# Performance work log

Measured on AMD Instinct MI355X. Metric: run time of the kernel, lower is better.

## Reference

```python
import jax, jax.numpy as jnp
import numpy as np

P, N, NF = 4, 871, 512            # num_meta_paths, node_size (hardcoded 871 in source), node_feature_size
XDIM = 116 * 116                   # x_proj input dim, hardcoded Linear(116*116, nf)
BETA, LAMBDA_WL, GAMMA = 0.1, 0.1, 0.1


def _xavier(k, shape):
    fan_in, fan_out = shape[0], shape[-1]
    bound = np.sqrt(6.0 / (fan_in + fan_out))
    return jax.random.uniform(k, shape, jnp.float32, -bound, bound)


def setup_inputs() -> dict:
    key = jax.random.key(0)
    ks = jax.random.split(key, 12)
    return {
        "z_stack": jax.random.normal(ks[0], (P, N, NF), jnp.float32),
        "x_orig": jax.random.normal(ks[1], (1, 116, 116), jnp.float32),
        "W": _xavier(ks[2], (N, 1)),
        "b": jax.random.uniform(ks[3], (N, 1), jnp.float32),
        "q": _xavier(ks[4], (N, NF)),
        "xp_w": _xavier(ks[5], (XDIM, NF)),
        "xp_b": jnp.zeros((NF,), jnp.float32),
        "w1": _xavier(ks[6], (2 * NF, 512)), "b1": jnp.zeros((512,), jnp.float32),
        "w2": _xavier(ks[7], (512, 256)), "b2": jnp.zeros((256,), jnp.float32),
        "w3": _xavier(ks[8], (256, 1)), "b3": jnp.zeros((1,), jnp.float32),
        "perm": jax.random.permutation(ks[9], N).astype(jnp.int32),
    }


def _mi_mlp(t, w1, b1, w2, b2, w3, b3):
    h = jax.nn.relu(t @ w1 + b1)
    h = jax.nn.relu(h @ w2 + b2)
    return h @ w3 + b3  # [N, 1]


def reference(z_stack, x_orig, W, b, q, xp_w, xp_b, w1, b1, w2, b2, w3, b3, perm):
    # --- vectorized form of the per-node loop:
    # score_p = mean_i( tanh(W_i * z[p,i,:] + b_i) . q_i )
    zt = jnp.tanh(W[None] * z_stack + b[None])            # [P,N,NF]
    scores = jnp.mean(jnp.sum(zt * q[None], axis=-1), axis=-1)  # [P]
    proportions = scores / jnp.sum(scores)
    attn = jax.nn.softmax(proportions)                    # [P] (no isomorphic pairs -> no overwrite)
    # layer_out_p = attn_p * z_p + z_p ; emb = sum_p layer_out_p
    emb = jnp.einsum('p,pnf->nf', 1.0 + attn, z_stack)    # [N,NF]
    # --- estimate_MI(x_orig, emb, mi_estimator_xz)
    x = jnp.broadcast_to(x_orig.reshape(1, -1), (N, XDIM))
    xh = x @ xp_w + xp_b                                  # [N,NF]
    t0 = jnp.concatenate([xh, emb], axis=1)               # [N,2NF]
    t1 = jnp.concatenate([xh, emb[perm]], axis=1)
    mi_lb = jnp.mean(_mi_mlp(t0, w1, b1, w2, b2, w3, b3)) - jnp.log(
        jnp.mean(jnp.exp(_mi_mlp(t1, w1, b1, w2, b2, w3, b3))) + 1e-8)
    I_XZ = jnp.clip(mi_lb, 0.0)
    # y_labels=None -> I_ZY = 0 ; empty isomorphic_pairs -> wl_loss = 0
    total_loss = I_XZ - BETA * 0.0 + LAMBDA_WL * 0.0 + GAMMA * jnp.sum(attn)
    return emb, total_loss
```

## Files before the change

### kernel.cpp

```cpp
#include <hip/hip_runtime.h>
#include <hip/hip_bf16.h>
#include <math.h>

#define NMETA  4
#define NNODE  871
#define NFEAT  512
#define XDIM   (116*116)
#define ZPLANE (NNODE*NFEAT)
#define NCHUNK 55
#define MT     55

#define WS_COEF   8
#define WS_CNT    12
#define WS_SPART  16
#define WS_C1P    256
#define WS_XHP    8448
#define WS_V      73984
#define WS_W1P    74856
#define WS_W2P    205928

typedef short v8s __attribute__((ext_vector_type(8)));
typedef float v4f __attribute__((ext_vector_type(4)));

static __device__ __forceinline__ short f2bf(float f) {
  __hip_bfloat16 h = __float2bfloat16(f);
  return *reinterpret_cast<short*>(&h);
}

__global__ __launch_bounds__(256) void k_front(const float* __restrict__ x,
                                               const float* __restrict__ xpw,
                                               const float* __restrict__ w1,
                                               const float* __restrict__ w2,
                                               const float* __restrict__ z,
                                               const float* __restrict__ W,
                                               const float* __restrict__ b,
                                               const float* __restrict__ q,
                                               float* __restrict__ ws,
                                               short* __restrict__ w1p,
                                               short* __restrict__ w2p) {
  const int blk = blockIdx.x;
  const int tid = threadIdx.x;
  if (blk < 128) {
    const int f4 = tid & 127;
    const int rp = tid >> 7;
    const int d0 = blk * 106;
    const int rows = min(106, XDIM - d0);
    __shared__ float xs[106];
    if (tid < rows) xs[tid] = x[d0 + tid];
    __syncthreads();
    float4 acc = {0.f, 0.f, 0.f, 0.f};
    const float4* xp4 = (const float4*)xpw;
#pragma unroll 4
    for (int r = rp; r < rows; r += 2) {
      const float xv = xs[r];
      const float4 w = xp4[(size_t)(d0 + r) * 128 + f4];
      acc.x += xv * w.x; acc.y += xv * w.y; acc.z += xv * w.z; acc.w += xv * w.w;
    }
    __shared__ float4 red4[128];
    if (rp) red4[f4] = acc;
    __syncthreads();
    if (!rp) {
      float4 o = red4[f4];
      o.x += acc.x; o.y += acc.y; o.z += acc.z; o.w += acc.w;
      ((float4*)(ws + WS_XHP + (size_t)blk * NFEAT))[f4] = o;
    }
  } else if (blk < 512) {
    const int base = (blk - 128) * 256 + tid;
#pragma unroll
    for (int it = 0; it < 4; ++it) {
      int t = base + it * 98304;
      if (t < 262144) {
        int j = t & 7; int r = t >> 3;
        int n15 = r & 15; r >>= 4;
        int quad = r & 3; r >>= 2;
        int nt = r & 31; int kb = r >> 5;
        int k = kb * 32 + quad * 8 + j;
        int n = nt * 16 + n15;
        w1p[t] = f2bf(w1[(size_t)(512 + k) * 512 + n]);
      } else {
        int o = t - 262144;
        int j = o & 7; int r = o >> 3;
        int n15 = r & 15; r >>= 4;
        int quad = r & 3; r >>= 2;
        int nt = r & 15; int kb = r >> 4;
        int k = kb * 32 + quad * 8 + j;
        int n = nt * 16 + n15;
        w2p[o] = f2bf(w2[(size_t)k * 256 + n]);
      }
    }
  } else {
    const int sblk = blk - 512;
    const int p = sblk / NCHUNK;
    const int chunk = sblk % NCHUNK;
    const int i0 = chunk * 16;
    const int i1 = min(i0 + 16, NNODE);
    const int f4 = tid & 127;
    const int ip = tid >> 7;
    float local = 0.f;
    for (int i = i0 + ip; i < i1; i += 2) {
      const float wi = W[i];
      const float bi = b[i];
      const float4 zr = ((const float4*)(z + ((size_t)p * NNODE + i) * NFEAT))[f4];
      const float4 qr = ((const float4*)(q + (size_t)i * NFEAT))[f4];
      local += tanhf(wi * zr.x + bi) * qr.x + tanhf(wi * zr.y + bi) * qr.y
             + tanhf(wi * zr.z + bi) * qr.z + tanhf(wi * zr.w + bi) * qr.w;
    }
    __shared__ float red[256];
    red[tid] = local;
    __syncthreads();
    for (int s = 128; s > 0; s >>= 1) {
      if (tid < s) red[tid] += red[tid + s];
      __syncthreads();
    }
    if (tid == 0) ws[WS_SPART + sblk] = red[0];
  }
}

__global__ __launch_bounds__(256) void k_prep(const float* __restrict__ xpb,
                                              const float* __restrict__ w1,
                                              const float* __restrict__ b1,
                                              float* __restrict__ ws) {
  const int tid = threadIdx.x;
  if (blockIdx.x < 16) {
    const int bk = blockIdx.x;
    __shared__ float xs[32];
    {
      const int f = tid & 31;
      const int pg = tid >> 5;
      float s = 0.f;
#pragma unroll 4
      for (int p = pg; p < 128; p += 8)
        s += ws[WS_XHP + (size_t)p * NFEAT + bk * 32 + f];
      __shared__ float red[256];
      red[tid] = s;
      __syncthreads();
      if (tid < 32) {
        float t2 = 0.f;
#pragma unroll
        for (int g = 0; g < 8; ++g) t2 += red[g * 32 + tid];
        xs[tid] = t2 + xpb[bk * 32 + tid];
      }
      __syncthreads();
    }
    const int j4 = tid & 127;
    const int fp = tid >> 7;
    float4 acc = {0.f, 0.f, 0.f, 0.f};
    const float4* w14 = (const float4*)w1;
#pragma unroll
    for (int ff = 0; ff < 16; ++ff) {
      const int f = bk * 32 + fp * 16 + ff;
      const float xv = xs[fp * 16 + ff];
      const float4 w = w14[(size_t)f * 128 + j4];
      acc.x += xv * w.x; acc.y += xv * w.y; acc.z += xv * w.z; acc.w += xv * w.w;
    }
    __shared__ float4 red2[128];
    if (fp) red2[j4] = acc;
    __syncthreads();
    if (!fp) {
      float4 o = red2[j4];
      o.x += acc.x; o.y += acc.y; o.z += acc.z; o.w += acc.w;
      if (bk == 0) {
        o.x += b1[j4 * 4 + 0]; o.y += b1[j4 * 4 + 1];
        o.z += b1[j4 * 4 + 2]; o.w += b1[j4 * 4 + 3];
      }
      ((float4*)(ws + WS_C1P + (size_t)bk * NFEAT))[j4] = o;
    }
  } else {
    __shared__ float sp[220];
    if (tid < 220) sp[tid] = ws[WS_SPART + tid];
    __syncthreads();
    if (tid == 0) {
      float sv[NMETA], sum = 0.f;
#pragma unroll
      for (int p = 0; p < NMETA; ++p) {
        float s = 0.f;
        for (int c = 0; c < NCHUNK; ++c) s += sp[p * NCHUNK + c];
        sv[p] = s / (float)NNODE;
        sum += sv[p];
      }
      float m = -1e30f;
#pragma unroll
      for (int p = 0; p < NMETA; ++p) { sv[p] = sv[p] / sum; m = fmaxf(m, sv[p]); }
      float es = 0.f;
#pragma unroll
      for (int p = 0; p < NMETA; ++p) { sv[p] = expf(sv[p] - m); es += sv[p]; }
#pragma unroll
      for (int p = 0; p < NMETA; ++p) ws[WS_COEF + p] = 1.f + sv[p] / es;
      *(unsigned int*)&ws[WS_CNT] = 0u;
    }
    for (int i = tid; i < NNODE; i += 256) ws[WS_V + i] = 0.f;
  }
}

__global__ __launch_bounds__(512) void k_fused(const float* __restrict__ z,
                                               float* __restrict__ ws,
                                               float* __restrict__ out,
                                               const short* __restrict__ w1p,
                                               const short* __restrict__ w2p,
                                               const float* __restrict__ b2,
                                               const float* __restrict__ w3,
                                               const float* __restrict__ b3) {
  __shared__ __align__(16) short embs[8192];
  __shared__ __align__(16) short h2a[8192];
  __shared__ float cs[512];
  __shared__ float rf0[512], rf1[512];
  const int tid = threadIdx.x;
  const int r0 = blockIdx.x * 16;

  {
    float a0 = 0.f;
#pragma unroll
    for (int k = 0; k < 16; ++k) a0 += ws[WS_C1P + k * 512 + tid];
    cs[tid] = a0;
  }
  const float c0 = ws[WS_COEF + 0], c1c = ws[WS_COEF + 1];
  const float c2 = ws[WS_COEF + 2], c3 = ws[WS_COEF + 3];

  const int oc = tid & 63;
  const float4* z4 = (const float4*)z;
  float4* out4 = (float4*)out;
#pragma unroll
  for (int t = 0; t < 2; ++t) {
    const int row = (tid >> 6) + 8 * t;
    const int gr = r0 + row;
    const int slot = oc * 16 + (row ^ (oc & 15));
    v8s h;
    if (gr < NNODE) {
      const int zi = gr * 128 + oc * 2;
      float4 a0 = z4[zi],               a1 = z4[zi + 1];
      float4 b0 = z4[NNODE*128 + zi],   b1 = z4[NNODE*128 + zi + 1];
      float4 d0 = z4[2*NNODE*128 + zi], d1 = z4[2*NNODE*128 + zi + 1];
      float4 e0 = z4[3*NNODE*128 + zi], e1 = z4[3*NNODE*128 + zi + 1];
      float4 r0v, r1v;
      r0v.x = c0*a0.x + c1c*b0.x + c2*d0.x + c3*e0.x;
      r0v.y = c0*a0.y + c1c*b0.y + c2*d0.y + c3*e0.y;
      r0v.z = c0*a0.z + c1c*b0.z + c2*d0.z + c3*e0.z;
      r0v.w = c0*a0.w + c1c*b0.w + c2*d0.w + c3*e0.w;
      r1v.x = c0*a1.x + c1c*b1.x + c2*d1.x + c3*e1.x;
      r1v.y = c0*a1.y + c1c*b1.y + c2*d1.y + c3*e1.y;
      r1v.z = c0*a1.z + c1c*b1.z + c2*d1.z + c3*e1.z;
      r1v.w = c0*a1.w + c1c*b1.w + c2*d1.w + c3*e1.w;
      out4[zi] = r0v;
      out4[zi + 1] = r1v;
      h[0] = f2bf(r0v.x); h[1] = f2bf(r0v.y); h[2] = f2bf(r0v.z); h[3] = f2bf(r0v.w);
      h[4] = f2bf(r1v.x); h[5] = f2bf(r1v.y); h[6] = f2bf(r1v.z); h[7] = f2bf(r1v.w);
    } else {
      h = (v8s){0,0,0,0,0,0,0,0};
    }
    *(v8s*)(embs + slot * 8) = h;
  }
  __syncthreads();

  const int lane = tid & 63, w = tid >> 6;
  const int n15 = lane & 15, quad = lane >> 4;
  v4f e[4];
#pragma unroll
  for (int ct = 0; ct < 4; ++ct) e[ct] = (v4f){0.f, 0.f, 0.f, 0.f};
#pragma unroll
  for (int kb = 0; kb < 16; ++kb) {
    const int koct = kb * 4 + quad;
    v8s a = *(const v8s*)(embs + (koct * 16 + (n15 ^ (koct & 15))) * 8);
    const short* B = w1p + kb * 16384 + w * 2048 + quad * 128 + n15 * 8;
#pragma unroll
    for (int ct = 0; ct < 4; ++ct) {
      v8s bb = *(const v8s*)(B + ct * 512);
      e[ct] = __builtin_amdgcn_mfma_f32_16x16x32_bf16(a, bb, e[ct], 0, 0, 0);
    }
  }
#pragma unroll
  for (int ct = 0; ct < 4; ++ct) {
    const int col = w * 64 + ct * 16 + n15;
    const int koct = col >> 3, j = col & 7;
#pragma unroll
    for (int r = 0; r < 4; ++r) {
      const int m = quad * 4 + r;
      h2a[(koct * 16 + (m ^ (koct & 15))) * 8 + j] = f2bf(fmaxf(e[ct][r] + cs[col], 0.f));
    }
  }
  __syncthreads();

  v4f g[2];
#pragma unroll
  for (int ct = 0; ct < 2; ++ct) g[ct] = (v4f){0.f, 0.f, 0.f, 0.f};
#pragma unroll
  for (int kb = 0; kb < 16; ++kb) {
    const int koct = kb * 4 + quad;
    v8s a = *(const v8s*)(h2a + (koct * 16 + (n15 ^ (koct & 15))) * 8);
    const short* B = w2p + kb * 8192 + w * 1024 + quad * 128 + n15 * 8;
#pragma unroll
    for (int ct = 0; ct < 2; ++ct) {
      v8s bb = *(const v8s*)(B + ct * 512);
      g[ct] = __builtin_amdgcn_mfma_f32_16x16x32_bf16(a, bb, g[ct], 0, 0, 0);
    }
  }
#pragma unroll
  for (int r = 0; r < 4; ++r) {
    float s = 0.f;
#pragma unroll
    for (int ct = 0; ct < 2; ++ct) {
      const int col = w * 32 + ct * 16 + n15;
      s += fmaxf(g[ct][r] + b2[col], 0.f) * w3[col];
    }
    s += __shfl_xor(s, 1);
    s += __shfl_xor(s, 2);
    s += __shfl_xor(s, 4);
    s += __shfl_xor(s, 8);
    const int grow = r0 + quad * 4 + r;
    if (n15 == 0 && grow < NNODE) atomicAdd(&ws[WS_V + grow], s);
  }

  __shared__ unsigned last;
  __syncthreads();
  if (tid == 0) {
    __threadfence();
    unsigned old = atomicAdd((unsigned int*)&ws[WS_CNT], 1u);
    last = (old == MT - 1) ? 1u : 0u;
  }
  __syncthreads();
  if (last) {
    const float bias = b3[0];
    float s0 = 0.f, s1 = 0.f;
    for (int i = tid; i < NNODE; i += 512) {
      float xv = __hip_atomic_load(&ws[WS_V + i], __ATOMIC_RELAXED,
                                   __HIP_MEMORY_SCOPE_AGENT) + bias;
      s0 += xv;
      s1 += expf(xv);
    }
    rf0[tid] = s0; rf1[tid] = s1;
    __syncthreads();
    for (int s = 256; s > 0; s >>= 1) {
      if (tid < s) { rf0[tid] += rf0[tid + s]; rf1[tid] += rf1[tid + s]; }
      __syncthreads();
    }
    if (tid == 0) {
      float m0 = rf0[0] / (float)NNODE;
      float m1 = rf1[0] / (float)NNODE;
      float mi = m0 - logf(m1 + 1e-8f);
      out[ZPLANE] = fmaxf(mi, 0.f) + 0.1f;
    }
  }
}

extern "C" void kernel_launch(void* const* d_in, const int* in_sizes, int n_in,
                              void* d_out, int out_size, void* d_ws, size_t ws_size,
                              hipStream_t stream) {
  const float* z   = (const float*)d_in[0];
  const float* x   = (const float*)d_in[1];
  const float* W   = (const float*)d_in[2];
  const float* b   = (const float*)d_in[3];
  const float* q   = (const float*)d_in[4];
  const float* xpw = (const float*)d_in[5];
  const float* xpb = (const float*)d_in[6];
  const float* w1  = (const float*)d_in[7];
  const float* b1  = (const float*)d_in[8];
  const float* w2  = (const float*)d_in[9];
  const float* b2  = (const float*)d_in[10];
  const float* w3  = (const float*)d_in[11];
  const float* b3  = (const float*)d_in[12];
  float* out = (float*)d_out;
  float* ws  = (float*)d_ws;

  short* w1p = (short*)(ws + WS_W1P);
  short* w2p = (short*)(ws + WS_W2P);

  k_front<<<732, 256, 0, stream>>>(x, xpw, w1, w2, z, W, b, q, ws, w1p, w2p);
  k_prep<<<17, 256, 0, stream>>>(xpb, w1, b1, ws);
  k_fused<<<MT, 512, 0, stream>>>(z, ws, out, w1p, w2p, b2, w3, b3);
}
```

Measured before the change: 131.9 us.

## Fold k_prep into k_fused, recomputing xh·w1 and attention per block

```diff
diff --git a/kernel.cpp b/kernel.cpp
--- a/kernel.cpp
+++ b/kernel.cpp
@@ -88,7 +88,7 @@
         w2p[o] = f2bf(w2[(size_t)k * 256 + n]);
       }
     }
-  } else {
+  } else if (blk < 732) {
     const int sblk = blk - 512;
     const int p = sblk / NCHUNK;
     const int chunk = sblk % NCHUNK;
@@ -113,82 +113,9 @@
       __syncthreads();
     }
     if (tid == 0) ws[WS_SPART + sblk] = red[0];
-  }
-}
-
-__global__ __launch_bounds__(256) void k_prep(const float* __restrict__ xpb,
-                                              const float* __restrict__ w1,
-                                              const float* __restrict__ b1,
-                                              float* __restrict__ ws) {
-  const int tid = threadIdx.x;
-  if (blockIdx.x < 16) {
-    const int bk = blockIdx.x;
-    __shared__ float xs[32];
-    {
-      const int f = tid & 31;
-      const int pg = tid >> 5;
-      float s = 0.f;
-#pragma unroll 4
-      for (int p = pg; p < 128; p += 8)
-        s += ws[WS_XHP + (size_t)p * NFEAT + bk * 32 + f];
-      __shared__ float red[256];
-      red[tid] = s;
-      __syncthreads();
-      if (tid < 32) {
-        float t2 = 0.f;
-#pragma unroll
-        for (int g = 0; g < 8; ++g) t2 += red[g * 32 + tid];
-        xs[tid] = t2 + xpb[bk * 32 + tid];
-      }
-      __syncthreads();
-    }
-    const int j4 = tid & 127;
-    const int fp = tid >> 7;
-    float4 acc = {0.f, 0.f, 0.f, 0.f};
-    const float4* w14 = (const float4*)w1;
-#pragma unroll
-    for (int ff = 0; ff < 16; ++ff) {
-      const int f = bk * 32 + fp * 16 + ff;
-      const float xv = xs[fp * 16 + ff];
-      const float4 w = w14[(size_t)f * 128 + j4];
-      acc.x += xv * w.x; acc.y += xv * w.y; acc.z += xv * w.z; acc.w += xv * w.w;
-    }
-    __shared__ float4 red2[128];
-    if (fp) red2[j4] = acc;
-    __syncthreads();
-    if (!fp) {
-      float4 o = red2[j4];
-      o.x += acc.x; o.y += acc.y; o.z += acc.z; o.w += acc.w;
-      if (bk == 0) {
-        o.x += b1[j4 * 4 + 0]; o.y += b1[j4 * 4 + 1];
-        o.z += b1[j4 * 4 + 2]; o.w += b1[j4 * 4 + 3];
-      }
-      ((float4*)(ws + WS_C1P + (size_t)bk * NFEAT))[j4] = o;
-    }
   } else {
-    __shared__ float sp[220];
-    if (tid < 220) sp[tid] = ws[WS_SPART + tid];
-    __syncthreads();
-    if (tid == 0) {
-      float sv[NMETA], sum = 0.f;
-#pragma unroll
-      for (int p = 0; p < NMETA; ++p) {
-        float s = 0.f;
-        for (int c = 0; c < NCHUNK; ++c) s += sp[p * NCHUNK + c];
-        sv[p] = s / (float)NNODE;
-        sum += sv[p];
-      }
-      float m = -1e30f;
-#pragma unroll
-      for (int p = 0; p < NMETA; ++p) { sv[p] = sv[p] / sum; m = fmaxf(m, sv[p]); }
-      float es = 0.f;
-#pragma unroll
-      for (int p = 0; p < NMETA; ++p) { sv[p] = expf(sv[p] - m); es += sv[p]; }
-#pragma unroll
-      for (int p = 0; p < NMETA; ++p) ws[WS_COEF + p] = 1.f + sv[p] / es;
-      *(unsigned int*)&ws[WS_CNT] = 0u;
-    }
     for (int i = tid; i < NNODE; i += 256) ws[WS_V + i] = 0.f;
+    if (tid == 0) *(unsigned int*)&ws[WS_CNT] = 0u;
   }
 }
 
@@ -199,22 +126,74 @@
                                                const short* __restrict__ w2p,
                                                const float* __restrict__ b2,
                                                const float* __restrict__ w3,
-                                               const float* __restrict__ b3) {
+                                               const float* __restrict__ b3,
+                                               const float* __restrict__ w1,
+                                               const float* __restrict__ b1,
+                                               const float* __restrict__ xpb) {
   __shared__ __align__(16) short embs[8192];
   __shared__ __align__(16) short h2a[8192];
   __shared__ float cs[512];
   __shared__ float rf0[512], rf1[512];
+  __shared__ float cf[4];
+  __shared__ float xs2[512];
+  __shared__ float spl[220];
+  __shared__ float4 redc[3][128];
   const int tid = threadIdx.x;
   const int r0 = blockIdx.x * 16;
 
+  if (tid < 220) spl[tid] = ws[WS_SPART + tid];
   {
-    float a0 = 0.f;
-#pragma unroll
-    for (int k = 0; k < 16; ++k) a0 += ws[WS_C1P + k * 512 + tid];
-    cs[tid] = a0;
-  }
-  const float c0 = ws[WS_COEF + 0], c1c = ws[WS_COEF + 1];
-  const float c2 = ws[WS_COEF + 2], c3 = ws[WS_COEF + 3];
+    float xv = xpb[tid];
+#pragma unroll 8
+    for (int p = 0; p < 128; ++p) xv += ws[WS_XHP + (size_t)p * NFEAT + tid];
+    xs2[tid] = xv;
+  }
+  __syncthreads();
+  if (tid == 0) {
+    float sv[NMETA], sum = 0.f;
+#pragma unroll
+    for (int p = 0; p < NMETA; ++p) {
+      float s = 0.f;
+      for (int c = 0; c < NCHUNK; ++c) s += spl[p * NCHUNK + c];
+      sv[p] = s / (float)NNODE;
+      sum += sv[p];
+    }
+    float m = -1e30f;
+#pragma unroll
+    for (int p = 0; p < NMETA; ++p) { sv[p] = sv[p] / sum; m = fmaxf(m, sv[p]); }
+    float es = 0.f;
+#pragma unroll
+    for (int p = 0; p < NMETA; ++p) { sv[p] = expf(sv[p] - m); es += sv[p]; }
+#pragma unroll
+    for (int p = 0; p < NMETA; ++p) cf[p] = 1.f + sv[p] / es;
+  }
+  const int j4 = tid & 127;
+  const int fp = tid >> 7;
+  float4 acc = {0.f, 0.f, 0.f, 0.f};
+  {
+    const float4* w14 = (const float4*)w1;
+#pragma unroll 4
+    for (int ff = 0; ff < 128; ++ff) {
+      const int f = fp * 128 + ff;
+      const float xvf = xs2[f];
+      const float4 wv = w14[(size_t)f * 128 + j4];
+      acc.x += xvf * wv.x; acc.y += xvf * wv.y; acc.z += xvf * wv.z; acc.w += xvf * wv.w;
+    }
+    if (fp) redc[fp - 1][j4] = acc;
+  }
+  __syncthreads();
+  if (!fp) {
+    float4 o = acc;
+#pragma unroll
+    for (int g = 0; g < 3; ++g) {
+      float4 t = redc[g][j4];
+      o.x += t.x; o.y += t.y; o.z += t.z; o.w += t.w;
+    }
+    o.x += b1[j4 * 4 + 0]; o.y += b1[j4 * 4 + 1];
+    o.z += b1[j4 * 4 + 2]; o.w += b1[j4 * 4 + 3];
+    ((float4*)cs)[j4] = o;
+  }
+  const float c0 = cf[0], c1c = cf[1], c2 = cf[2], c3 = cf[3];
 
   const int oc = tid & 63;
   const float4* z4 = (const float4*)z;
@@ -228,7 +207,7 @@
     if (gr < NNODE) {
       const int zi = gr * 128 + oc * 2;
       float4 a0 = z4[zi],               a1 = z4[zi + 1];
-      float4 b0 = z4[NNODE*128 + zi],   b1 = z4[NNODE*128 + zi + 1];
+      float4 b0 = z4[NNODE*128 + zi],   b1v = z4[NNODE*128 + zi + 1];
       float4 d0 = z4[2*NNODE*128 + zi], d1 = z4[2*NNODE*128 + zi + 1];
       float4 e0 = z4[3*NNODE*128 + zi], e1 = z4[3*NNODE*128 + zi + 1];
       float4 r0v, r1v;
@@ -236,10 +215,10 @@
       r0v.y = c0*a0.y + c1c*b0.y + c2*d0.y + c3*e0.y;
       r0v.z = c0*a0.z + c1c*b0.z + c2*d0.z + c3*e0.z;
       r0v.w = c0*a0.w + c1c*b0.w + c2*d0.w + c3*e0.w;
-      r1v.x = c0*a1.x + c1c*b1.x + c2*d1.x + c3*e1.x;
-      r1v.y = c0*a1.y + c1c*b1.y + c2*d1.y + c3*e1.y;
-      r1v.z = c0*a1.z + c1c*b1.z + c2*d1.z + c3*e1.z;
-      r1v.w = c0*a1.w + c1c*b1.w + c2*d1.w + c3*e1.w;
+      r1v.x = c0*a1.x + c1c*b1v.x + c2*d1.x + c3*e1.x;
+      r1v.y = c0*a1.y + c1c*b1v.y + c2*d1.y + c3*e1.y;
+      r1v.z = c0*a1.z + c1c*b1v.z + c2*d1.z + c3*e1.z;
+      r1v.w = c0*a1.w + c1c*b1v.w + c2*d1.w + c3*e1.w;
       out4[zi] = r0v;
       out4[zi + 1] = r1v;
       h[0] = f2bf(r0v.x); h[1] = f2bf(r0v.y); h[2] = f2bf(r0v.z); h[3] = f2bf(r0v.w);
@@ -363,7 +342,6 @@
   short* w1p = (short*)(ws + WS_W1P);
   short* w2p = (short*)(ws + WS_W2P);
 
-  k_front<<<732, 256, 0, stream>>>(x, xpw, w1, w2, z, W, b, q, ws, w1p, w2p);
-  k_prep<<<17, 256, 0, stream>>>(xpb, w1, b1, ws);
-  k_fused<<<MT, 512, 0, stream>>>(z, ws, out, w1p, w2p, b2, w3, b3);
+  k_front<<<733, 256, 0, stream>>>(x, xpw, w1, w2, z, W, b, q, ws, w1p, w2p);
+  k_fused<<<MT, 512, 0, stream>>>(z, ws, out, w1p, w2p, b2, w3, b3, w1, b1, xpb);
 }
```

Result: slower. 146.3 us (+10.9%).
